# Performance work log

Measured on AMD Instinct MI355X. Metric: run time of the kernel, lower is better.

## Reference

```python
import jax, jax.numpy as jnp
import numpy as np

BETA = 0.25  # commitment loss weight (init kwarg)


def setup_inputs() -> dict:
    key = jax.random.key(0)
    k1, k2 = jax.random.split(key)
    z = jax.random.normal(k1, (16, 256, 32, 32), dtype=jnp.float32)
    embedding = jax.random.normal(k2, (8192, 256), dtype=jnp.float32)
    return {"z": z, "embedding": embedding}


def reference(z, embedding):
    # z: [B, C, H, W]  embedding: [K, C]
    B, C, H, W = z.shape
    zp = jnp.transpose(z, (0, 2, 3, 1))            # [B, H, W, C]
    zf = zp.reshape(-1, C)                          # [N, C]
    # squared euclidean distances via ||z||^2 + ||e||^2 - 2 z.e : [N, K]
    d = (jnp.sum(zf * zf, axis=1, keepdims=True)
         + jnp.sum(embedding * embedding, axis=1)
         - 2.0 * jnp.einsum('nd,kd->nk', zf, embedding))
    min_encoding_indices = jnp.argmin(d, axis=1)    # [N]
    z_q = embedding[min_encoding_indices].reshape(zp.shape)  # [B, H, W, C]
    loss = (BETA * jnp.mean((jax.lax.stop_gradient(z_q) - zp) ** 2)
            + jnp.mean((z_q - jax.lax.stop_gradient(zp)) ** 2))
    # straight-through estimator
    z_q = zp + jax.lax.stop_gradient(z_q - zp)
    z_q = jnp.transpose(z_q, (0, 3, 1, 2))          # back to [B, C, H, W]
    return z_q, loss, min_encoding_indices
```

## Files before the change

### kernel.cpp

```cpp
#include <hip/hip_runtime.h>

typedef unsigned int u32;
typedef unsigned long long u64;

#define C_DIM 256
#define HW 1024
#define N_TOT 16384
#define K_DIM 8192
#define ZQ_SIZE 4194304
#define LOSS_OFF ZQ_SIZE
#define IDX_OFF (ZQ_SIZE + 1)

#define KRANGE 2048
#define MARGIN 2.0f
#define CAP 524288u
#define LCAP 8192u

#define WS_ENORM 0
#define WS_CNT 8192
#define WS_PACKED 16384
#define WS_FIDX 49152
#define WS_LPART 65536
#define WS_LIST 131072
#define WS_ZT32 1179648
#define WS_ZTB16 5373952
#define WS_EB16 7471104

typedef __attribute__((ext_vector_type(4))) float f32x4;
typedef __attribute__((ext_vector_type(8))) __bf16 bf16x8;
typedef __attribute__((ext_vector_type(8))) unsigned short u16x8;

__device__ __forceinline__ void gld_lds16(const void* g, void* l) {
    __builtin_amdgcn_global_load_lds(
        (const __attribute__((address_space(1))) u32*)g,
        (__attribute__((address_space(3))) u32*)l, 16, 0, 0);
}

__device__ __forceinline__ bf16x8 gload16(const void* p) {
    bf16x8 r;
    asm volatile("global_load_dwordx4 %0, %1, off" : "=v"(r) : "v"(p));
    return r;
}

__device__ __forceinline__ unsigned short f2bf(float f) {
    u32 u = __float_as_uint(f);
    u32 r = (u + 0x7FFFu + ((u >> 16) & 1u)) >> 16;
    return (unsigned short)r;
}

__global__ __launch_bounds__(256) void k_prep_e(const float* __restrict__ e,
                                                unsigned short* __restrict__ eb,
                                                float* __restrict__ enorm1) {
    int w = threadIdx.x >> 6, l = threadIdx.x & 63;
    int row = blockIdx.x * 4 + w;
    const float4 v = *reinterpret_cast<const float4*>(e + (size_t)row * C_DIM + l * 4);
    float s = v.x * v.x + v.y * v.y + v.z * v.z + v.w * v.w;
    #pragma unroll
    for (int off = 32; off; off >>= 1) s += __shfl_xor(s, off, 64);
    if (l == 0) enorm1[row] = s + 1024.0f;
    ushort4 h;
    h.x = f2bf(v.x); h.y = f2bf(v.y); h.z = f2bf(v.z); h.w = f2bf(v.w);
    *reinterpret_cast<ushort4*>(eb + (size_t)row * C_DIM + l * 4) = h;
}

__global__ __launch_bounds__(256) void k_prep_z(const float* __restrict__ z,
                                                float* __restrict__ zt32,
                                                unsigned short* __restrict__ ztb) {
    int bid = blockIdx.x;
    int b = bid >> 7;
    int hwt = (bid >> 3) & 15;
    int ct = bid & 7;
    int t = threadIdx.x;
    __shared__ float tile[32][65];
    #pragma unroll
    for (int p = 0; p < 8; ++p) {
        int cl = p * 4 + (t >> 6), hl = t & 63;
        tile[cl][hl] = z[((size_t)b << 18) + ((size_t)(ct * 32 + cl) << 10) + hwt * 64 + hl];
    }
    __syncthreads();
    int hl = t & 63, cg = t >> 6;
    int n = (b << 10) + hwt * 64 + hl;
    float v[8];
    #pragma unroll
    for (int j = 0; j < 8; ++j) v[j] = tile[cg * 8 + j][hl];
    size_t base = (size_t)n * C_DIM + ct * 32 + cg * 8;
    *reinterpret_cast<float4*>(zt32 + base) = make_float4(v[0], v[1], v[2], v[3]);
    *reinterpret_cast<float4*>(zt32 + base + 4) = make_float4(v[4], v[5], v[6], v[7]);
    u16x8 h;
    #pragma unroll
    for (int j = 0; j < 8; ++j) h[j] = f2bf(v[j]);
    *reinterpret_cast<u16x8*>(ztb + base) = h;
}

__global__ __launch_bounds__(256, 2) void k_screen(const unsigned short* __restrict__ zt,
                                                   const unsigned short* __restrict__ et,
                                                   const float* __restrict__ enorm1,
                                                   u32* __restrict__ cnt,
                                                   uint2* __restrict__ list) {
    __shared__ __align__(16) char lds[67088];
    char* Bb = lds;

    int logical = (blockIdx.x & 7) * 64 + (blockIdx.x >> 3);
    const int ks = logical >> 7;
    const int rowtile = logical & 127;
    const int n0 = rowtile * 128;
    const int kbase = ks * KRANGE;

    const int tid = threadIdx.x;
    const int l = tid & 63, w = tid >> 6;
    const int wr = w >> 1, wc = w & 1;
    const int ll = l & 15, lh = l >> 4;

    const char* srcB[2];
    char* dstB[2];
    #pragma unroll
    for (int j = 0; j < 2; ++j) {
        int D = w * 128 + j * 64 + l;
        int rB = D >> 2;
        int sB = (D & 3) ^ ((rB >> 1) & 3);
        srcB[j] = (const char*)et + ((size_t)(kbase + rB) << 9) + (sB << 4);
        dstB[j] = Bb + (w * 128 + j * 64) * 16;
    }
    int bfrOff[4];
    #pragma unroll
    for (int kf = 0; kf < 4; ++kf) {
        int row = wc * 64 + kf * 16 + ll;
        bfrOff[kf] = (row * 4 + (lh ^ ((row >> 1) & 3))) * 16;
    }

    gld_lds16(srcB[0], dstB[0]);
    gld_lds16(srcB[1], dstB[1]);

    const char* abase = (const char*)zt + (((size_t)(n0 + wr * 64 + ll)) << 9) + lh * 16;
    bf16x8 afr[4][8];
    #pragma unroll
    for (int mf = 0; mf < 4; ++mf)
        #pragma unroll
        for (int q = 0; q < 8; ++q)
            afr[mf][q] = gload16(abase + mf * 8192 + q * 64);
    asm volatile("s_waitcnt vmcnt(0)" ::: "memory");
    __builtin_amdgcn_sched_barrier(0);

    f32x4 acc[4][4];
    #pragma unroll
    for (int a = 0; a < 4; ++a)
        #pragma unroll
        for (int b = 0; b < 4; ++b) acc[a][b] = (f32x4){0.f, 0.f, 0.f, 0.f};
    float m1[16], m2[16];
    #pragma unroll
    for (int s = 0; s < 16; ++s) { m1[s] = 3.4e38f; m2[s] = 3.4e38f; }

    __syncthreads();

    for (int it = 0; it < 16; ++it) {
        float en[4];
        #pragma unroll
        for (int kf = 0; kf < 4; ++kf)
            en[kf] = enorm1[kbase + it * 128 + wc * 64 + kf * 16 + ll];

        #pragma unroll
        for (int cs = 0; cs < 8; ++cs) {
            const int p = cs & 1;
            if (it < 15 || cs < 7) {
                const size_t koff = (size_t)it * 65536 + ((cs == 7) ? 65536 : (cs + 1) * 64);
                gld_lds16(srcB[0] + koff, dstB[0] + (p ^ 1) * 8192);
                gld_lds16(srcB[1] + koff, dstB[1] + (p ^ 1) * 8192);
            }
            bf16x8 bfr[4];
            #pragma unroll
            for (int kf = 0; kf < 4; ++kf)
                bfr[kf] = *reinterpret_cast<const bf16x8*>(Bb + p * 8192 + bfrOff[kf]);
            __builtin_amdgcn_s_setprio(1);
            #pragma unroll
            for (int mf = 0; mf < 4; ++mf)
                #pragma unroll
                for (int kf = 0; kf < 4; ++kf)
                    acc[mf][kf] = __builtin_amdgcn_mfma_f32_16x16x32_bf16(
                        afr[mf][cs], bfr[kf], acc[mf][kf], 0, 0, 0);
            __builtin_amdgcn_s_setprio(0);

            if (cs == 7) {
                #pragma unroll
                for (int kf = 0; kf < 4; ++kf) {
                    const u32 kcol = (u32)(kbase + it * 128 + wc * 64 + kf * 16 + ll);
                    #pragma unroll
                    for (int mf = 0; mf < 4; ++mf) {
                        #pragma unroll
                        for (int r = 0; r < 4; ++r) {
                            float d = fmaf(-2.0f, acc[mf][kf][r], en[kf]);
                            float df = __uint_as_float((__float_as_uint(d) & 0xFFFFE000u) | kcol);
                            const int s2 = mf * 4 + r;
                            float t = fmaxf(m1[s2], df);
                            m2[s2] = fminf(m2[s2], t);
                            m1[s2] = fminf(m1[s2], df);
                            acc[mf][kf][r] = 0.0f;
                        }
                    }
                }
            }
            __syncthreads();
        }
    }

    float rowm[16];
    #pragma unroll
    for (int s = 0; s < 16; ++s) rowm[s] = m1[s];
    #pragma unroll
    for (int m = 1; m <= 8; m <<= 1)
        #pragma unroll
        for (int s = 0; s < 16; ++s)
            rowm[s] = fminf(rowm[s], __shfl_xor(rowm[s], m, 64));

    float* LDSrm = (float*)(lds + 65536);
    float* LDSrmF = (float*)(lds + 66560);
    u32* ccnt = (u32*)(lds + 67072);
    u32* gbase = (u32*)(lds + 67076);
    uint2* cbuf = (uint2*)lds;

    if (ll == 0) {
        #pragma unroll
        for (int s = 0; s < 16; ++s) {
            int row_local = wr * 64 + (s >> 2) * 16 + lh * 4 + (s & 3);
            LDSrm[row_local * 2 + wc] = rowm[s];
        }
    }
    if (tid == 0) *ccnt = 0;
    __syncthreads();
    if (tid < 128)
        LDSrmF[tid] = fminf(LDSrm[tid * 2], LDSrm[tid * 2 + 1]);
    __syncthreads();

    #pragma unroll
    for (int s = 0; s < 16; ++s) {
        int row_local = wr * 64 + (s >> 2) * 16 + lh * 4 + (s & 3);
        float rm = __uint_as_float(__float_as_uint(LDSrmF[row_local]) & 0xFFFFE000u);
        float d1 = __uint_as_float(__float_as_uint(m1[s]) & 0xFFFFE000u);
        if (d1 <= rm + MARGIN) {
            u32 pos = atomicAdd(ccnt, 1u);
            uint2 ent = make_uint2((u32)(n0 + row_local), __float_as_uint(m1[s]) & 8191u);
            if (pos < LCAP) cbuf[pos] = ent;
            else { u32 gp = atomicAdd(cnt, 1u); if (gp < CAP) list[gp] = ent; }
        }
        float d2 = __uint_as_float(__float_as_uint(m2[s]) & 0xFFFFE000u);
        if (d2 <= rm + MARGIN) {
            for (int it2 = 0; it2 < 16; ++it2) {
                #pragma unroll
                for (int kf = 0; kf < 4; ++kf) {
                    u32 k = (u32)(kbase + it2 * 128 + wc * 64 + kf * 16 + ll);
                    u32 pos = atomicAdd(ccnt, 1u);
                    uint2 ent = make_uint2((u32)(n0 + row_local), k);
                    if (pos < LCAP) cbuf[pos] = ent;
                    else { u32 gp = atomicAdd(cnt, 1u); if (gp < CAP) list[gp] = ent; }
                }
            }
        }
    }
    __syncthreads();
    if (tid == 0) {
        u32 total = *ccnt; if (total > LCAP) total = LCAP;
        *gbase = atomicAdd(cnt, total);
    }
    __syncthreads();
    u32 total = *ccnt; if (total > LCAP) total = LCAP;
    u32 gb = *gbase;
    for (u32 i = tid; i < total; i += 256) {
        u32 gp = gb + i;
        if (gp < CAP) list[gp] = cbuf[i];
    }
}

__global__ __launch_bounds__(256) void k_exact(const float* __restrict__ zt32,
                                               const float* __restrict__ e,
                                               const float* __restrict__ enorm1,
                                               const u32* __restrict__ cnt,
                                               const uint2* __restrict__ list,
                                               u64* __restrict__ packed) {
    const int nw = gridDim.x * 4;
    const int wid = blockIdx.x * 4 + (threadIdx.x >> 6);
    const int l = threadIdx.x & 63;
    u32 total = *cnt;
    if (total > CAP) total = CAP;
    for (u32 i = wid; i < total; i += nw) {
        uint2 c = list[i];
        const float4 zv = *reinterpret_cast<const float4*>(zt32 + (size_t)c.x * C_DIM + l * 4);
        const float4 ev = *reinterpret_cast<const float4*>(e + (size_t)c.y * C_DIM + l * 4);
        float s = zv.x * ev.x + zv.y * ev.y + zv.z * ev.z + zv.w * ev.w;
        #pragma unroll
        for (int off = 32; off; off >>= 1) s += __shfl_xor(s, off, 64);
        if (l == 0) {
            float d = fmaf(-2.0f, s, enorm1[c.y]);
            u32 ub = __float_as_uint(d);
            ub = (ub & 0x80000000u) ? ~ub : (ub | 0x80000000u);
            u64 key = ((u64)ub << 32) | (u64)c.y;
            atomicMin(packed + c.x, key);
        }
    }
}

__global__ __launch_bounds__(256) void k_fin(const u64* __restrict__ packed,
                                             int* __restrict__ fidx,
                                             float* __restrict__ out_idx) {
    int n = blockIdx.x * 256 + threadIdx.x;
    if (n >= N_TOT) return;
    u32 kk = (u32)(packed[n] & 0xFFFFFFFFull);
    if (kk > 8191u) kk = 0u;
    fidx[n] = (int)kk;
    out_idx[n] = (float)kk;
}

#define GBLOCKS 2048
__global__ __launch_bounds__(256) void k_gather(const float* __restrict__ z,
                                                const float* __restrict__ e,
                                                const int* __restrict__ fidx,
                                                float* __restrict__ zq,
                                                float* __restrict__ lpart) {
    float s = 0.0f;
    for (int i = blockIdx.x * 256 + threadIdx.x; i < ZQ_SIZE; i += GBLOCKS * 256) {
        int bb = i >> 18;
        int c = (i >> 10) & 255;
        int hw = i & 1023;
        int n = (bb << 10) | hw;
        float q = e[(size_t)fidx[n] * C_DIM + c];
        float zv = z[i];
        zq[i] = q;
        float d = q - zv;
        s = fmaf(d, d, s);
    }
    #pragma unroll
    for (int off = 32; off; off >>= 1) s += __shfl_xor(s, off, 64);
    __shared__ float wsum[4];
    int lane = threadIdx.x & 63, w = threadIdx.x >> 6;
    if (lane == 0) wsum[w] = s;
    __syncthreads();
    if (threadIdx.x == 0) lpart[blockIdx.x] = wsum[0] + wsum[1] + wsum[2] + wsum[3];
}

__global__ __launch_bounds__(256) void k_loss(const float* __restrict__ lpart,
                                              float* __restrict__ out_loss) {
    float s = 0.0f;
    for (int i = threadIdx.x; i < GBLOCKS; i += 256) s += lpart[i];
    #pragma unroll
    for (int off = 32; off; off >>= 1) s += __shfl_xor(s, off, 64);
    __shared__ float wsum[4];
    int lane = threadIdx.x & 63, w = threadIdx.x >> 6;
    if (lane == 0) wsum[w] = s;
    __syncthreads();
    if (threadIdx.x == 0)
        out_loss[0] = (wsum[0] + wsum[1] + wsum[2] + wsum[3]) * (1.25f / (float)ZQ_SIZE);
}

extern "C" void kernel_launch(void* const* d_in, const int* in_sizes, int n_in,
                              void* d_out, int out_size, void* d_ws, size_t ws_size,
                              hipStream_t stream) {
    const float* z = (const float*)d_in[0];
    const float* e = (const float*)d_in[1];
    float* out = (float*)d_out;
    float* ws = (float*)d_ws;

    float* enorm1 = ws + WS_ENORM;
    u32* cnt = (u32*)(ws + WS_CNT);
    u64* packed = (u64*)(ws + WS_PACKED);
    int* fidx = (int*)(ws + WS_FIDX);
    float* lpart = ws + WS_LPART;
    uint2* list = (uint2*)(ws + WS_LIST);
    float* zt32 = ws + WS_ZT32;
    unsigned short* ztb = (unsigned short*)(ws + WS_ZTB16);
    unsigned short* eb = (unsigned short*)(ws + WS_EB16);

    hipMemsetAsync(cnt, 0, sizeof(u32), stream);
    hipMemsetAsync(packed, 0xFF, (size_t)N_TOT * sizeof(u64), stream);

    k_prep_e<<<dim3(K_DIM / 4), dim3(256), 0, stream>>>(e, eb, enorm1);
    k_prep_z<<<dim3(2048), dim3(256), 0, stream>>>(z, zt32, ztb);
    k_screen<<<dim3(512), dim3(256), 0, stream>>>(ztb, eb, enorm1, cnt, list);
    k_exact<<<dim3(1024), dim3(256), 0, stream>>>(zt32, e, enorm1, cnt, list, packed);
    k_fin<<<dim3(64), dim3(256), 0, stream>>>(packed, fidx, out + IDX_OFF);
    k_gather<<<dim3(GBLOCKS), dim3(256), 0, stream>>>(z, e, fidx, out, lpart);
    k_loss<<<dim3(1), dim3(256), 0, stream>>>(lpart, out + LOSS_OFF);
}
```

Baseline: 227.9 us.

## Stage second half of A fragments in swizzled LDS to cut register pressure

The screening kernel now holds only the first half of each A-row fragment (channels 0-127) in registers and loads the second half into a swizzled LDS buffer, reading it per K-step for cs>=4. The inline-asm global loads and explicit waitcnt barrier are replaced by plain loads. LDS per block shrinks, LCAP halves, and launch bounds drop to min 1 block per SM. The aim is to reduce VGPR usage and free scheduling freedom, at the cost of extra LDS reads inside the MFMA loop and possibly lower guaranteed occupancy.

```diff
diff --git a/kernel.cpp b/kernel.cpp
--- a/kernel.cpp
+++ b/kernel.cpp
@@ -14,7 +14,7 @@
 #define KRANGE 2048
 #define MARGIN 2.0f
 #define CAP 524288u
-#define LCAP 8192u
+#define LCAP 4096u
 
 #define WS_ENORM 0
 #define WS_CNT 8192
@@ -36,12 +36,6 @@
         (__attribute__((address_space(3))) u32*)l, 16, 0, 0);
 }
 
-__device__ __forceinline__ bf16x8 gload16(const void* p) {
-    bf16x8 r;
-    asm volatile("global_load_dwordx4 %0, %1, off" : "=v"(r) : "v"(p));
-    return r;
-}
-
 __device__ __forceinline__ unsigned short f2bf(float f) {
     u32 u = __float_as_uint(f);
     u32 r = (u + 0x7FFFu + ((u >> 16) & 1u)) >> 16;
@@ -92,13 +86,14 @@
     *reinterpret_cast<u16x8*>(ztb + base) = h;
 }
 
-__global__ __launch_bounds__(256, 2) void k_screen(const unsigned short* __restrict__ zt,
+__global__ __launch_bounds__(256, 1) void k_screen(const unsigned short* __restrict__ zt,
                                                    const unsigned short* __restrict__ et,
                                                    const float* __restrict__ enorm1,
                                                    u32* __restrict__ cnt,
                                                    uint2* __restrict__ list) {
-    __shared__ __align__(16) char lds[67088];
-    char* Bb = lds;
+    __shared__ __align__(16) char lds[50704];
+    char* Ab2 = lds;
+    char* Bb = lds + 32768;
 
     int logical = (blockIdx.x & 7) * 64 + (blockIdx.x >> 3);
     const int ks = logical >> 7;
@@ -110,6 +105,16 @@
     const int l = tid & 63, w = tid >> 6;
     const int wr = w >> 1, wc = w & 1;
     const int ll = l & 15, lh = l >> 4;
+
+    #pragma unroll
+    for (int j = 0; j < 8; ++j) {
+        int Y = (w * 8 + j) * 1024 + l * 16;
+        int row = Y >> 8;
+        int slot = (Y >> 4) & 15;
+        const char* src = (const char*)zt + (((size_t)(n0 + row)) << 9) + 256
+                          + ((slot ^ (row & 7)) << 4);
+        gld_lds16(src, Ab2 + (w * 8 + j) * 1024);
+    }
 
     const char* srcB[2];
     char* dstB[2];
@@ -127,19 +132,24 @@
         int row = wc * 64 + kf * 16 + ll;
         bfrOff[kf] = (row * 4 + (lh ^ ((row >> 1) & 3))) * 16;
     }
+    int a2off[4], rx2[4];
+    #pragma unroll
+    for (int mf = 0; mf < 4; ++mf) {
+        int row = wr * 64 + mf * 16 + ll;
+        a2off[mf] = row * 256;
+        rx2[mf] = row & 7;
+    }
 
     gld_lds16(srcB[0], dstB[0]);
     gld_lds16(srcB[1], dstB[1]);
 
     const char* abase = (const char*)zt + (((size_t)(n0 + wr * 64 + ll)) << 9) + lh * 16;
-    bf16x8 afr[4][8];
+    bf16x8 afr[4][4];
     #pragma unroll
     for (int mf = 0; mf < 4; ++mf)
         #pragma unroll
-        for (int q = 0; q < 8; ++q)
-            afr[mf][q] = gload16(abase + mf * 8192 + q * 64);
-    asm volatile("s_waitcnt vmcnt(0)" ::: "memory");
-    __builtin_amdgcn_sched_barrier(0);
+        for (int q = 0; q < 4; ++q)
+            afr[mf][q] = *reinterpret_cast<const bf16x8*>(abase + mf * 8192 + q * 64);
 
     f32x4 acc[4][4];
     #pragma unroll
@@ -170,13 +180,22 @@
             #pragma unroll
             for (int kf = 0; kf < 4; ++kf)
                 bfr[kf] = *reinterpret_cast<const bf16x8*>(Bb + p * 8192 + bfrOff[kf]);
+            bf16x8 af[4];
+            #pragma unroll
+            for (int mf = 0; mf < 4; ++mf) {
+                if (cs < 4)
+                    af[mf] = afr[mf][cs];
+                else
+                    af[mf] = *reinterpret_cast<const bf16x8*>(
+                        Ab2 + a2off[mf] + ((((cs - 4) * 4 + lh) ^ rx2[mf]) << 4));
+            }
             __builtin_amdgcn_s_setprio(1);
             #pragma unroll
             for (int mf = 0; mf < 4; ++mf)
                 #pragma unroll
                 for (int kf = 0; kf < 4; ++kf)
                     acc[mf][kf] = __builtin_amdgcn_mfma_f32_16x16x32_bf16(
-                        afr[mf][cs], bfr[kf], acc[mf][kf], 0, 0, 0);
+                        af[mf], bfr[kf], acc[mf][kf], 0, 0, 0);
             __builtin_amdgcn_s_setprio(0);
 
             if (cs == 7) {
@@ -211,10 +230,10 @@
         for (int s = 0; s < 16; ++s)
             rowm[s] = fminf(rowm[s], __shfl_xor(rowm[s], m, 64));
 
-    float* LDSrm = (float*)(lds + 65536);
-    float* LDSrmF = (float*)(lds + 66560);
-    u32* ccnt = (u32*)(lds + 67072);
-    u32* gbase = (u32*)(lds + 67076);
+    float* LDSrm = (float*)(lds + 49152);
+    float* LDSrmF = (float*)(lds + 50176);
+    u32* ccnt = (u32*)(lds + 50688);
+    u32* gbase = (u32*)(lds + 50692);
     uint2* cbuf = (uint2*)lds;
 
     if (ll == 0) {
```

Result: slower. 239.9 us (+5.3%).
